# Optimization experiments

Measured on AMD Instinct MI355X. Metric: run time of the kernel, lower is better.

Reference implementation:

```python
import jax, jax.numpy as jnp
import numpy as np

B, S, D, KC = 32, 4096, 64, 256  # batch*heads, seq_len, head_dim, compressed dim


def setup_inputs() -> dict:
    key = jax.random.key(0)
    ks = jax.random.split(key, 7)
    return {
        "Q": jax.random.normal(ks[0], (B, S, D), dtype=jnp.float32),
        "K": jax.random.normal(ks[1], (B, S, D), dtype=jnp.float32),
        "V": jax.random.normal(ks[2], (B, S, D), dtype=jnp.float32),
        "E_w": jax.random.normal(ks[3], (KC, S), dtype=jnp.float32) * (1.0 / np.sqrt(S)),
        "E_b": jax.random.normal(ks[4], (KC,), dtype=jnp.float32) * 0.01,
        "F_w": jax.random.normal(ks[5], (KC, S), dtype=jnp.float32) * (1.0 / np.sqrt(S)),
        "F_b": jax.random.normal(ks[6], (KC,), dtype=jnp.float32) * 0.01,
    }


def reference(Q, K, V, E_w, E_b, F_w, F_b):
    # K: [B,S,D] -> transpose -> [B,D,S]; E proj over seq axis -> [B,D,KC]
    Ke = jnp.einsum("bsd,ks->bdk", K, E_w) + E_b  # [B, D, KC]
    # scores: Q @ E(K) -> [B, S, KC], scaled by sqrt(head_dim)
    scale = jnp.sqrt(jnp.asarray(D, dtype=Q.dtype))
    P = jnp.einsum("bsd,bdk->bsk", Q, Ke) / scale
    # causal mask: torch.triu(ones(S, KC)) keeps (i, j) where j >= i
    i = jnp.arange(S)[:, None]
    j = jnp.arange(KC)[None, :]
    keep = j >= i  # [S, KC]
    P = jnp.where(keep[None, :, :], P, jnp.asarray(-1e10, dtype=P.dtype))
    P = jax.nn.softmax(P, axis=-1)  # dropout p=0.0 -> identity
    # V: [B,S,D] -> [B,D,S]; F proj -> [B,D,KC]; transpose -> [B,KC,D]
    Vf = jnp.einsum("bsd,ks->bkd", V, F_w) + F_b[None, :, None]  # [B, KC, D]
    out = jnp.einsum("bsk,bkd->bsd", P, Vf)  # [B, S, D]
    return out
```

## Files before the change

kernel.cpp:

```cpp
#include <hip/hip_runtime.h>
#include <hip/hip_bf16.h>
#include <math.h>

#define NB  32
#define NS  4096
#define ND  64
#define NKC 256
#define ASTR 72
#define PBSTR 264
#define VSTR  264

typedef __attribute__((ext_vector_type(8))) short short8;
typedef __attribute__((ext_vector_type(4))) float f32x4;

__device__ __forceinline__ short f2bf(float f) {
    union { float f; unsigned u; } v; v.f = f;
    return (short)((v.u + 0x7FFFu + ((v.u >> 16) & 1u)) >> 16);
}

__global__ __launch_bounds__(256, 4) void proj_gemm(
    const float* __restrict__ Ew, const float* __restrict__ Fw,
    const float* __restrict__ K,  const float* __restrict__ V,
    float* __restrict__ part)
{
    const int x = blockIdx.x, y = blockIdx.y;
    const int chunk = x >> 1, mm = x & 1;
    const int b = y >> 1, mhalf = y & 1;
    const float* __restrict__ A  = (mm ? Fw : Ew) + (size_t)(mhalf * 128) * NS;
    const float* __restrict__ Bg = mm ? V : K;
    float* __restrict__ Pout = part + ((size_t)x * 32 + b) * 16384 + mhalf * 8192;

    const int t = threadIdx.x, wave = t >> 6, lane = t & 63;
    const int lm = lane & 15, g = lane >> 4;
    __shared__ short As[128 * ASTR];
    __shared__ short Bs[64 * ASTR];
    const size_t bBase = (size_t)b * NS * ND;
    const int rA = t >> 3, jA = t & 7;
    const int dB = t & 31, sB = t >> 5;

    f32x4 acc[2][4];
#pragma unroll
    for (int mt = 0; mt < 2; ++mt)
#pragma unroll
        for (int nt = 0; nt < 4; ++nt) acc[mt][nt] = (f32x4){0.f, 0.f, 0.f, 0.f};

    const int sBeg = chunk * 512, sEnd = sBeg + 512;
    float4 paf[8];
    float2 pb[8];
#pragma unroll
    for (int i = 0; i < 4; ++i) {
        paf[2 * i]     = *(const float4*)&A[(size_t)(i * 32 + rA) * NS + sBeg + jA * 8];
        paf[2 * i + 1] = *(const float4*)&A[(size_t)(i * 32 + rA) * NS + sBeg + jA * 8 + 4];
    }
#pragma unroll
    for (int i = 0; i < 8; ++i)
        pb[i] = *(const float2*)&Bg[bBase + (size_t)(sBeg + sB * 8 + i) * ND + dB * 2];

    for (int s0 = sBeg; s0 < sEnd; s0 += 64) {
#pragma unroll
        for (int i = 0; i < 4; ++i) {
            short8 w;
            w[0] = f2bf(paf[2 * i].x);     w[1] = f2bf(paf[2 * i].y);
            w[2] = f2bf(paf[2 * i].z);     w[3] = f2bf(paf[2 * i].w);
            w[4] = f2bf(paf[2 * i + 1].x); w[5] = f2bf(paf[2 * i + 1].y);
            w[6] = f2bf(paf[2 * i + 1].z); w[7] = f2bf(paf[2 * i + 1].w);
            *(short8*)&As[(i * 32 + rA) * ASTR + jA * 8] = w;
        }
        {
            short8 w0, w1;
#pragma unroll
            for (int i = 0; i < 8; ++i) { w0[i] = f2bf(pb[i].x); w1[i] = f2bf(pb[i].y); }
            *(short8*)&Bs[(dB * 2 + 0) * ASTR + sB * 8] = w0;
            *(short8*)&Bs[(dB * 2 + 1) * ASTR + sB * 8] = w1;
        }
        __syncthreads();
        if (s0 + 64 < sEnd) {
#pragma unroll
            for (int i = 0; i < 4; ++i) {
                paf[2 * i]     = *(const float4*)&A[(size_t)(i * 32 + rA) * NS + s0 + 64 + jA * 8];
                paf[2 * i + 1] = *(const float4*)&A[(size_t)(i * 32 + rA) * NS + s0 + 64 + jA * 8 + 4];
            }
#pragma unroll
            for (int i = 0; i < 8; ++i)
                pb[i] = *(const float2*)&Bg[bBase + (size_t)(s0 + 64 + sB * 8 + i) * ND + dB * 2];
        }
#pragma unroll
        for (int ks = 0; ks < 64; ks += 32) {
            short8 aF[2];
#pragma unroll
            for (int mt = 0; mt < 2; ++mt)
                aF[mt] = *(const short8*)&As[(mt * 64 + wave * 16 + lm) * ASTR + ks + g * 8];
#pragma unroll
            for (int nt = 0; nt < 4; ++nt) {
                short8 bF = *(const short8*)&Bs[(nt * 16 + lm) * ASTR + ks + g * 8];
#pragma unroll
                for (int mt = 0; mt < 2; ++mt)
                    acc[mt][nt] = __builtin_amdgcn_mfma_f32_16x16x32_bf16(aF[mt], bF, acc[mt][nt], 0, 0, 0);
            }
        }
        __syncthreads();
    }
#pragma unroll
    for (int mt = 0; mt < 2; ++mt)
#pragma unroll
        for (int r = 0; r < 4; ++r) {
            int kcl = mt * 64 + wave * 16 + g * 4 + r;
#pragma unroll
            for (int nt = 0; nt < 4; ++nt)
                Pout[kcl * 64 + nt * 16 + lm] = acc[mt][nt][r];
        }
}

__global__ __launch_bounds__(256) void reduce_part(
    const float* __restrict__ part, float* __restrict__ KeT, float* __restrict__ Vf)
{
    const int x = blockIdx.x, y = blockIdx.y, t = threadIdx.x;
    const int b = y >> 1, mm = y & 1;
    float* __restrict__ Out = (mm ? Vf : KeT) + (size_t)b * NKC * ND;

    const int kc = x * 32 + (t >> 3);
    const int dO = (t & 7) * 8;
    const int mhalf = kc >> 7, kcl = kc & 127;
    const size_t inner = (size_t)mhalf * 8192 + kcl * 64 + dO;

    float4 s0 = (float4){0.f, 0.f, 0.f, 0.f};
    float4 s1 = (float4){0.f, 0.f, 0.f, 0.f};
#pragma unroll
    for (int c = 0; c < 8; ++c) {
        const float* p = part + ((size_t)(c * 2 + mm) * 32 + b) * 16384 + inner;
        float4 a = *(const float4*)p, bb = *(const float4*)(p + 4);
        s0.x += a.x;  s0.y += a.y;  s0.z += a.z;  s0.w += a.w;
        s1.x += bb.x; s1.y += bb.y; s1.z += bb.z; s1.w += bb.w;
    }
    *(float4*)&Out[(size_t)kc * 64 + dO]     = s0;
    *(float4*)&Out[(size_t)kc * 64 + dO + 4] = s1;
}

__global__ __launch_bounds__(256) void attn_fused(
    const float* __restrict__ Q,  const float* __restrict__ KeT,
    const float* __restrict__ Vf, const float* __restrict__ Eb,
    const float* __restrict__ Fb, float* __restrict__ out)
{
    const int x = blockIdx.x, b = blockIdx.y, t = threadIdx.x;

    if (x >= 8) {
        __shared__ float pq[16][64];
        __shared__ float mv[64];
        const int kg = t >> 4, dq = t & 15;
        float4 s4 = (float4){0.f, 0.f, 0.f, 0.f};
        for (int p = 0; p < 16; ++p) {
            int k = p * 16 + kg;
            float4 v = *(const float4*)&Vf[((size_t)b * NKC + k) * ND + dq * 4];
            float fb = Fb[k];
            s4.x += v.x + fb; s4.y += v.y + fb; s4.z += v.z + fb; s4.w += v.w + fb;
        }
        *(float4*)&pq[kg][dq * 4] = s4;
        __syncthreads();
        if (t < 64) {
            float m = 0.f;
#pragma unroll
            for (int i = 0; i < 16; ++i) m += pq[i][t];
            mv[t] = m * (1.f / 256.f);
        }
        __syncthreads();
        const int r0 = 256 + (x - 8) * 64;
#pragma unroll
        for (int i = 0; i < 4; ++i) {
            int idx = i * 256 + t, row = idx >> 4, q = idx & 15;
            *(float4*)&out[((size_t)b * NS + r0 + row) * ND + q * 4] =
                *(const float4*)&mv[q * 4];
        }
        return;
    }

    const int s0 = x * 32;
    const int wave = t >> 6, lane = t & 63, lm = lane & 15, g = lane >> 4;
    __shared__ short Qs[32 * ASTR];
    __shared__ short PsB[32 * PBSTR];
    __shared__ short VfT[64 * VSTR];
    __shared__ float rsums[32][4];

    {
        int row = t >> 3, dq = t & 7;
        size_t off = ((size_t)b * NS + s0 + row) * ND + dq * 8;
        float4 q0 = *(const float4*)&Q[off], q1 = *(const float4*)&Q[off + 4];
        short8 w;
        w[0] = f2bf(q0.x); w[1] = f2bf(q0.y); w[2] = f2bf(q0.z); w[3] = f2bf(q0.w);
        w[4] = f2bf(q1.x); w[5] = f2bf(q1.y); w[6] = f2bf(q1.z); w[7] = f2bf(q1.w);
        *(short8*)&Qs[row * ASTR + dq * 8] = w;
    }
    {
        const int dB = t & 31, sB = t >> 5;
#pragma unroll
        for (int pass = 0; pass < 4; ++pass) {
            int kb = pass * 64 + sB * 8;
            float2 v[8]; float fb[8];
#pragma unroll
            for (int i = 0; i < 8; ++i) {
                v[i]  = *(const float2*)&Vf[((size_t)b * NKC + kb + i) * ND + dB * 2];
                fb[i] = Fb[kb + i];
            }
            short8 w0, w1;
#pragma unroll
            for (int i = 0; i < 8; ++i) {
                w0[i] = f2bf(v[i].x + fb[i]);
                w1[i] = f2bf(v[i].y + fb[i]);
            }
            *(short8*)&VfT[(dB * 2 + 0) * VSTR + kb] = w0;
            *(short8*)&VfT[(dB * 2 + 1) * VSTR + kb] = w1;
        }
    }
    __syncthreads();

    f32x4 accP[2][4];
#pragma unroll
    for (int rt = 0; rt < 2; ++rt)
#pragma unroll
        for (int kk = 0; kk < 4; ++kk) accP[rt][kk] = (f32x4){0.f, 0.f, 0.f, 0.f};
#pragma unroll
    for (int kk = 0; kk < 4; ++kk) {
        int kt = wave * 4 + kk;
        float ebv = Eb[kt * 16 + lm];
#pragma unroll
        for (int ks2 = 0; ks2 < 2; ++ks2) {
            const float* kp = &KeT[((size_t)b * NKC + kt * 16 + lm) * ND + ks2 * 32 + g * 8];
            float4 c0 = *(const float4*)kp, c1 = *(const float4*)(kp + 4);
            short8 bf;
            bf[0] = f2bf(c0.x + ebv); bf[1] = f2bf(c0.y + ebv);
            bf[2] = f2bf(c0.z + ebv); bf[3] = f2bf(c0.w + ebv);
            bf[4] = f2bf(c1.x + ebv); bf[5] = f2bf(c1.y + ebv);
            bf[6] = f2bf(c1.z + ebv); bf[7] = f2bf(c1.w + ebv);
#pragma unroll
            for (int rt = 0; rt < 2; ++rt) {
                short8 aq = *(const short8*)&Qs[(rt * 16 + lm) * ASTR + ks2 * 32 + g * 8];
                accP[rt][kk] = __builtin_amdgcn_mfma_f32_16x16x32_bf16(aq, bf, accP[rt][kk], 0, 0, 0);
            }
        }
    }
#pragma unroll
    for (int rt = 0; rt < 2; ++rt)
#pragma unroll
        for (int r = 0; r < 4; ++r) {
            float s = 0.f;
            int rowg = s0 + rt * 16 + g * 4 + r;
#pragma unroll
            for (int kk = 0; kk < 4; ++kk) {
                int col = wave * 64 + kk * 16 + lm;
                float e = (col >= rowg) ? __expf(accP[rt][kk][r] * 0.125f) : 0.f;
                accP[rt][kk][r] = e;
                s += e;
            }
#pragma unroll
            for (int off = 1; off <= 8; off <<= 1) s += __shfl_xor(s, off, 64);
            if (lm == 0) rsums[rt * 16 + g * 4 + r][wave] = s;
        }
    __syncthreads();
#pragma unroll
    for (int rt = 0; rt < 2; ++rt)
#pragma unroll
        for (int r = 0; r < 4; ++r) {
            float4 rs = *(const float4*)&rsums[rt * 16 + g * 4 + r][0];
            float inv = 1.f / (rs.x + rs.y + rs.z + rs.w);
#pragma unroll
            for (int kk = 0; kk < 4; ++kk)
                PsB[(rt * 16 + g * 4 + r) * PBSTR + wave * 64 + kk * 16 + lm] =
                    f2bf(accP[rt][kk][r] * inv);
        }
    __syncthreads();

    f32x4 oa[2];
    oa[0] = (f32x4){0.f, 0.f, 0.f, 0.f};
    oa[1] = (f32x4){0.f, 0.f, 0.f, 0.f};
    for (int ks = x; ks < 8; ++ks) {
        short8 bv = *(const short8*)&VfT[(wave * 16 + lm) * VSTR + ks * 32 + g * 8];
#pragma unroll
        for (int rt = 0; rt < 2; ++rt) {
            short8 av = *(const short8*)&PsB[(rt * 16 + lm) * PBSTR + ks * 32 + g * 8];
            oa[rt] = __builtin_amdgcn_mfma_f32_16x16x32_bf16(av, bv, oa[rt], 0, 0, 0);
        }
    }
#pragma unroll
    for (int rt = 0; rt < 2; ++rt)
#pragma unroll
        for (int r = 0; r < 4; ++r)
            out[((size_t)b * NS + s0 + rt * 16 + g * 4 + r) * ND + wave * 16 + lm] = oa[rt][r];
}

extern "C" void kernel_launch(void* const* d_in, const int* in_sizes, int n_in,
                              void* d_out, int out_size, void* d_ws, size_t ws_size,
                              hipStream_t stream) {
    (void)in_sizes; (void)n_in; (void)out_size; (void)ws_size;
    const float* Q  = (const float*)d_in[0];
    const float* K  = (const float*)d_in[1];
    const float* V  = (const float*)d_in[2];
    const float* Ew = (const float*)d_in[3];
    const float* Eb = (const float*)d_in[4];
    const float* Fw = (const float*)d_in[5];
    const float* Fb = (const float*)d_in[6];
    float* out = (float*)d_out;

    const size_t nKe = (size_t)NB * NKC * ND;
    float* KeT = (float*)d_ws;
    float* Vf  = KeT + nKe;

    proj_gemm<<<dim3(16, 64), 256, 0, stream>>>(Ew, Fw, K, V, out);
    reduce_part<<<dim3(8, 64), 256, 0, stream>>>(out, KeT, Vf);
    attn_fused<<<dim3(68, NB), 256, 0, stream>>>(Q, KeT, Vf, Eb, Fb, out);
}
```

Measured before the change: 181.0 us.

## Replace split-K partial buffer and reduce kernel with atomic accumulation

```diff
diff --git a/kernel.cpp b/kernel.cpp
--- a/kernel.cpp
+++ b/kernel.cpp
@@ -11,6 +11,7 @@
 #define VSTR  264
 
 typedef __attribute__((ext_vector_type(8))) short short8;
+typedef __attribute__((ext_vector_type(4))) short sv4;
 typedef __attribute__((ext_vector_type(4))) float f32x4;
 
 __device__ __forceinline__ short f2bf(float f) {
@@ -18,122 +19,89 @@
     return (short)((v.u + 0x7FFFu + ((v.u >> 16) & 1u)) >> 16);
 }
 
-__global__ __launch_bounds__(256, 4) void proj_gemm(
+__global__ __launch_bounds__(256, 8) void proj_gemm(
     const float* __restrict__ Ew, const float* __restrict__ Fw,
     const float* __restrict__ K,  const float* __restrict__ V,
-    float* __restrict__ part)
+    float* __restrict__ KeT, float* __restrict__ Vf)
 {
     const int x = blockIdx.x, y = blockIdx.y;
     const int chunk = x >> 1, mm = x & 1;
-    const int b = y >> 1, mhalf = y & 1;
-    const float* __restrict__ A  = (mm ? Fw : Ew) + (size_t)(mhalf * 128) * NS;
+    const int b = y >> 2, mt = y & 3;
+    const float* __restrict__ A  = (mm ? Fw : Ew) + (size_t)(mt * 64) * NS;
     const float* __restrict__ Bg = mm ? V : K;
-    float* __restrict__ Pout = part + ((size_t)x * 32 + b) * 16384 + mhalf * 8192;
+    float* __restrict__ Cout     = (mm ? Vf : KeT) + (size_t)b * NKC * ND;
 
     const int t = threadIdx.x, wave = t >> 6, lane = t & 63;
     const int lm = lane & 15, g = lane >> 4;
-    __shared__ short As[128 * ASTR];
+    __shared__ short As[64 * ASTR];
     __shared__ short Bs[64 * ASTR];
     const size_t bBase = (size_t)b * NS * ND;
-    const int rA = t >> 3, jA = t & 7;
-    const int dB = t & 31, sB = t >> 5;
-
-    f32x4 acc[2][4];
-#pragma unroll
-    for (int mt = 0; mt < 2; ++mt)
-#pragma unroll
-        for (int nt = 0; nt < 4; ++nt) acc[mt][nt] = (f32x4){0.f, 0.f, 0.f, 0.f};
+    const int rA = t >> 4, qA = t & 15;
+    const int sq = t >> 4, dq = t & 15;
+
+    f32x4 acc[4];
+#pragma unroll
+    for (int nt = 0; nt < 4; ++nt) acc[nt] = (f32x4){0.f, 0.f, 0.f, 0.f};
 
     const int sBeg = chunk * 512, sEnd = sBeg + 512;
-    float4 paf[8];
-    float2 pb[8];
-#pragma unroll
-    for (int i = 0; i < 4; ++i) {
-        paf[2 * i]     = *(const float4*)&A[(size_t)(i * 32 + rA) * NS + sBeg + jA * 8];
-        paf[2 * i + 1] = *(const float4*)&A[(size_t)(i * 32 + rA) * NS + sBeg + jA * 8 + 4];
-    }
-#pragma unroll
-    for (int i = 0; i < 8; ++i)
-        pb[i] = *(const float2*)&Bg[bBase + (size_t)(sBeg + sB * 8 + i) * ND + dB * 2];
+    float4 paf[4];
+    float4 pbf[4];
+#pragma unroll
+    for (int i = 0; i < 4; ++i)
+        paf[i] = *(const float4*)&A[(size_t)(i * 16 + rA) * NS + sBeg + qA * 4];
+#pragma unroll
+    for (int j = 0; j < 4; ++j)
+        pbf[j] = *(const float4*)&Bg[bBase + (size_t)(sBeg + sq * 4 + j) * ND + dq * 4];
 
     for (int s0 = sBeg; s0 < sEnd; s0 += 64) {
 #pragma unroll
         for (int i = 0; i < 4; ++i) {
-            short8 w;
-            w[0] = f2bf(paf[2 * i].x);     w[1] = f2bf(paf[2 * i].y);
-            w[2] = f2bf(paf[2 * i].z);     w[3] = f2bf(paf[2 * i].w);
-            w[4] = f2bf(paf[2 * i + 1].x); w[5] = f2bf(paf[2 * i + 1].y);
-            w[6] = f2bf(paf[2 * i + 1].z); w[7] = f2bf(paf[2 * i + 1].w);
-            *(short8*)&As[(i * 32 + rA) * ASTR + jA * 8] = w;
+            sv4 w;
+            w.x = f2bf(paf[i].x); w.y = f2bf(paf[i].y);
+            w.z = f2bf(paf[i].z); w.w = f2bf(paf[i].w);
+            *(sv4*)&As[(i * 16 + rA) * ASTR + qA * 4] = w;
         }
         {
-            short8 w0, w1;
-#pragma unroll
-            for (int i = 0; i < 8; ++i) { w0[i] = f2bf(pb[i].x); w1[i] = f2bf(pb[i].y); }
-            *(short8*)&Bs[(dB * 2 + 0) * ASTR + sB * 8] = w0;
-            *(short8*)&Bs[(dB * 2 + 1) * ASTR + sB * 8] = w1;
+            float vv[4][4] = {
+                {pbf[0].x, pbf[0].y, pbf[0].z, pbf[0].w},
+                {pbf[1].x, pbf[1].y, pbf[1].z, pbf[1].w},
+                {pbf[2].x, pbf[2].y, pbf[2].z, pbf[2].w},
+                {pbf[3].x, pbf[3].y, pbf[3].z, pbf[3].w}};
+#pragma unroll
+            for (int jd = 0; jd < 4; ++jd) {
+                sv4 w;
+                w.x = f2bf(vv[0][jd]); w.y = f2bf(vv[1][jd]);
+                w.z = f2bf(vv[2][jd]); w.w = f2bf(vv[3][jd]);
+                *(sv4*)&Bs[(dq * 4 + jd) * ASTR + sq * 4] = w;
+            }
         }
         __syncthreads();
         if (s0 + 64 < sEnd) {
 #pragma unroll
-            for (int i = 0; i < 4; ++i) {
-                paf[2 * i]     = *(const float4*)&A[(size_t)(i * 32 + rA) * NS + s0 + 64 + jA * 8];
-                paf[2 * i + 1] = *(const float4*)&A[(size_t)(i * 32 + rA) * NS + s0 + 64 + jA * 8 + 4];
-            }
-#pragma unroll
-            for (int i = 0; i < 8; ++i)
-                pb[i] = *(const float2*)&Bg[bBase + (size_t)(s0 + 64 + sB * 8 + i) * ND + dB * 2];
+            for (int i = 0; i < 4; ++i)
+                paf[i] = *(const float4*)&A[(size_t)(i * 16 + rA) * NS + s0 + 64 + qA * 4];
+#pragma unroll
+            for (int j = 0; j < 4; ++j)
+                pbf[j] = *(const float4*)&Bg[bBase + (size_t)(s0 + 64 + sq * 4 + j) * ND + dq * 4];
         }
 #pragma unroll
         for (int ks = 0; ks < 64; ks += 32) {
-            short8 aF[2];
-#pragma unroll
-            for (int mt = 0; mt < 2; ++mt)
-                aF[mt] = *(const short8*)&As[(mt * 64 + wave * 16 + lm) * ASTR + ks + g * 8];
+            short8 aF = *(const short8*)&As[(wave * 16 + lm) * ASTR + ks + g * 8];
 #pragma unroll
             for (int nt = 0; nt < 4; ++nt) {
                 short8 bF = *(const short8*)&Bs[(nt * 16 + lm) * ASTR + ks + g * 8];
-#pragma unroll
-                for (int mt = 0; mt < 2; ++mt)
-                    acc[mt][nt] = __builtin_amdgcn_mfma_f32_16x16x32_bf16(aF[mt], bF, acc[mt][nt], 0, 0, 0);
-            }
-        }
-        __syncthreads();
-    }
-#pragma unroll
-    for (int mt = 0; mt < 2; ++mt)
-#pragma unroll
-        for (int r = 0; r < 4; ++r) {
-            int kcl = mt * 64 + wave * 16 + g * 4 + r;
-#pragma unroll
-            for (int nt = 0; nt < 4; ++nt)
-                Pout[kcl * 64 + nt * 16 + lm] = acc[mt][nt][r];
-        }
-}
-
-__global__ __launch_bounds__(256) void reduce_part(
-    const float* __restrict__ part, float* __restrict__ KeT, float* __restrict__ Vf)
-{
-    const int x = blockIdx.x, y = blockIdx.y, t = threadIdx.x;
-    const int b = y >> 1, mm = y & 1;
-    float* __restrict__ Out = (mm ? Vf : KeT) + (size_t)b * NKC * ND;
-
-    const int kc = x * 32 + (t >> 3);
-    const int dO = (t & 7) * 8;
-    const int mhalf = kc >> 7, kcl = kc & 127;
-    const size_t inner = (size_t)mhalf * 8192 + kcl * 64 + dO;
-
-    float4 s0 = (float4){0.f, 0.f, 0.f, 0.f};
-    float4 s1 = (float4){0.f, 0.f, 0.f, 0.f};
-#pragma unroll
-    for (int c = 0; c < 8; ++c) {
-        const float* p = part + ((size_t)(c * 2 + mm) * 32 + b) * 16384 + inner;
-        float4 a = *(const float4*)p, bb = *(const float4*)(p + 4);
-        s0.x += a.x;  s0.y += a.y;  s0.z += a.z;  s0.w += a.w;
-        s1.x += bb.x; s1.y += bb.y; s1.z += bb.z; s1.w += bb.w;
-    }
-    *(float4*)&Out[(size_t)kc * 64 + dO]     = s0;
-    *(float4*)&Out[(size_t)kc * 64 + dO + 4] = s1;
+                acc[nt] = __builtin_amdgcn_mfma_f32_16x16x32_bf16(aF, bF, acc[nt], 0, 0, 0);
+            }
+        }
+        __syncthreads();
+    }
+#pragma unroll
+    for (int r = 0; r < 4; ++r) {
+        int kc = mt * 64 + wave * 16 + g * 4 + r;
+#pragma unroll
+        for (int nt = 0; nt < 4; ++nt)
+            atomicAdd(&Cout[(size_t)kc * ND + nt * 16 + lm], acc[nt][r]);
+    }
 }
 
 __global__ __launch_bounds__(256) void attn_fused(
@@ -303,7 +271,7 @@
     float* KeT = (float*)d_ws;
     float* Vf  = KeT + nKe;
 
-    proj_gemm<<<dim3(16, 64), 256, 0, stream>>>(Ew, Fw, K, V, out);
-    reduce_part<<<dim3(8, 64), 256, 0, stream>>>(out, KeT, Vf);
+    hipMemsetAsync(d_ws, 0, 2 * nKe * sizeof(float), stream);
+    proj_gemm<<<dim3(16, 128), 256, 0, stream>>>(Ew, Fw, K, V, KeT, Vf);
     attn_fused<<<dim3(68, NB), 256, 0, stream>>>(Q, KeT, Vf, Eb, Fb, out);
 }
```

Result: slower. 241.9 us (+33.6%).
